# Optimization experiments

Measured on AMD Instinct MI355X. Metric: run time of the kernel, lower is better.

## Reference

```python
import jax, jax.numpy as jnp
import numpy as np

N, NF, INF, NHID = 8192, 128, 128, 16


def _gcn(x, adj, dis, W, b):
    # GraphConvolution: support = x @ W; aggregate with distance-weighted adjacency
    support = x @ W  # [N, out]
    return (adj * dis) @ support + b


def setup_inputs() -> dict:
    key = jax.random.key(0)
    ks = jax.random.split(key, 26)

    def lin(k, i, o):
        kw, kb = jax.random.split(k)
        W = jax.random.uniform(kw, (i, o), jnp.float32, -1.0, 1.0) / np.sqrt(i).astype(np.float32)
        b = jax.random.uniform(kb, (o,), jnp.float32, -1.0, 1.0) / np.sqrt(i).astype(np.float32)
        return W, b

    x = jax.random.normal(ks[0], (N, NF), jnp.float32)
    adj = jax.random.uniform(ks[1], (N, N), jnp.float32)
    dis = jax.random.uniform(ks[2], (N, N), jnp.float32)

    W1, b1 = lin(ks[3], NF, NF)        # linear1
    Wg1, bg1 = lin(ks[4], NF, INF)     # gc1
    Wm1, bm1 = lin(ks[5], INF, 64)     # linear_med1
    Wm2, bm2 = lin(ks[6], 64, 128)     # linear_med2
    Wm3, bm3 = lin(ks[7], 128, 64)     # linear_med3
    Wm4, bm4 = lin(ks[8], 64, 64)      # linear_med4
    Wgh, bgh = lin(ks[9], 64, 64)      # gconv_hidden[0]
    W2, b2 = lin(ks[10], 64, 32)       # linear2
    Wg2, bg2 = lin(ks[11], 32, 32)     # gc2
    W3, b3 = lin(ks[12], 32, NHID)     # linear3

    return dict(x=x, adj=adj, dis=dis, W1=W1, b1=b1, Wg1=Wg1, bg1=bg1,
                Wm1=Wm1, bm1=bm1, Wm2=Wm2, bm2=bm2, Wm3=Wm3, bm3=bm3,
                Wm4=Wm4, bm4=bm4, Wgh=Wgh, bgh=bgh, W2=W2, b2=b2,
                Wg2=Wg2, bg2=bg2, W3=W3, b3=b3)


def reference(x, adj, dis, W1, b1, Wg1, bg1, Wm1, bm1, Wm2, bm2, Wm3, bm3,
              Wm4, bm4, Wgh, bgh, W2, b2, Wg2, bg2, W3, b3):
    lrelu = lambda v: jax.nn.leaky_relu(v, 0.2)
    x0 = _gcn(x @ W1 + b1, adj, dis, Wg1, bg1)
    x0 = lrelu(x0 @ Wm1 + bm1)
    x0 = lrelu(x0 @ Wm2 + bm2)
    x0 = lrelu(x0 @ Wm3 + bm3)
    x0 = jax.nn.relu(x0 @ Wm4 + bm4)
    x_res = x0
    x0 = jax.nn.relu(_gcn(x0, adj, dis, Wgh, bgh) + x_res)  # one hidden gconv layer
    x0 = x0 @ W2 + b2
    x0 = _gcn(x0, adj, dis, Wg2, bg2)
    return x0 @ W3 + b3
```

## Files before the change

kernel.cpp:

```cpp
#include <hip/hip_runtime.h>
#include <hip/hip_bf16.h>

#define NROWS 8192
typedef unsigned short u16;
typedef short bf16x8 __attribute__((ext_vector_type(8)));
typedef short bf16x4 __attribute__((ext_vector_type(4)));
typedef float f32x4 __attribute__((ext_vector_type(4)));

__device__ __forceinline__ u16 f2b(float f) {
    unsigned u = __float_as_uint(f);
    unsigned r = (u + 0x7fffu + ((u >> 16) & 1u)) >> 16;
    return (u16)r;
}
__device__ __forceinline__ float b2f(u16 v) {
    return __uint_as_float(((unsigned)v) << 16);
}

template<int MODE> __device__ __forceinline__ float actf(float v) {
    if constexpr (MODE == 1) return fmaxf(v, 0.f);
    else if constexpr (MODE == 2) return v > 0.f ? v : 0.2f * v;
    else return v;
}

__global__ __launch_bounds__(256) void fold1(
    const float* __restrict__ W1, const float* __restrict__ b1,
    const float* __restrict__ Wg1,
    const float* __restrict__ W2, const float* __restrict__ b2,
    const float* __restrict__ Wg2, float* __restrict__ ws) {
    float* T2 = ws + 9376;
    float* v1 = ws + 11424;
    float* v2 = ws + 11552;
    float* T1 = ws + 16384;
    const int tid = threadIdx.x, b = blockIdx.x;
    if (b < 16) {
        int i = b * 8 + (tid >> 5), j4 = (tid & 31) << 2;
        float4 acc = {0, 0, 0, 0};
        for (int k = 0; k < 128; ++k) {
            float a = W1[i * 128 + k];
            float4 g = *(const float4*)&Wg1[k * 128 + j4];
            acc.x += a * g.x; acc.y += a * g.y; acc.z += a * g.z; acc.w += a * g.w;
        }
        *(float4*)&T1[i * 128 + j4] = acc;
    } else if (b == 16) {
        if (tid < 128) {
            float s = 0;
            for (int k = 0; k < 128; ++k) s += b1[k] * Wg1[k * 128 + tid];
            v1[tid] = s;
        } else if (tid < 160) {
            int j = tid - 128;
            float s = 0;
            for (int k = 0; k < 32; ++k) s += b2[k] * Wg2[k * 32 + j];
            v2[j] = s;
        }
    } else {
        for (int o4 = tid; o4 < 64 * 8; o4 += 256) {
            int i = o4 >> 3, j4 = (o4 & 7) << 2;
            float4 acc = {0, 0, 0, 0};
            for (int k = 0; k < 32; ++k) {
                float a = W2[i * 32 + k];
                float4 g = *(const float4*)&Wg2[k * 32 + j4];
                acc.x += a * g.x; acc.y += a * g.y; acc.z += a * g.z; acc.w += a * g.w;
            }
            *(float4*)&T2[i * 32 + j4] = acc;
        }
    }
}

__global__ __launch_bounds__(256) void fold2(
    const float* __restrict__ Wm1, const float* __restrict__ bm1,
    const float* __restrict__ bg1,
    const float* __restrict__ W3, const float* __restrict__ b3,
    const float* __restrict__ bg2, float* __restrict__ ws) {
    float* WA = ws + 0;
    float* bA = ws + 8192;
    float* cA = ws + 8256;
    float* WB = ws + 8320;
    float* bB = ws + 9344;
    float* cB = ws + 9360;
    const float* T2 = ws + 9376;
    const float* v1 = ws + 11424;
    const float* v2 = ws + 11552;
    const float* T1 = ws + 16384;
    const int tid = threadIdx.x, b = blockIdx.x;
    if (b < 8) {
        int i = b * 16 + (tid >> 4), j4 = (tid & 15) << 2;
        float4 acc = {0, 0, 0, 0};
        for (int k = 0; k < 128; ++k) {
            float a = T1[i * 128 + k];
            float4 g = *(const float4*)&Wm1[k * 64 + j4];
            acc.x += a * g.x; acc.y += a * g.y; acc.z += a * g.z; acc.w += a * g.w;
        }
        *(float4*)&WA[i * 64 + j4] = acc;
    } else if (b == 8) {
        if (tid < 64) {
            float s = 0, c = 0;
            for (int k = 0; k < 128; ++k) {
                s += v1[k] * Wm1[k * 64 + tid];
                c += bg1[k] * Wm1[k * 64 + tid];
            }
            bA[tid] = s; cA[tid] = c + bm1[tid];
        } else if (tid < 80) {
            int j = tid - 64;
            float s = 0, c = 0;
            for (int k = 0; k < 32; ++k) {
                s += v2[k] * W3[k * 16 + j];
                c += bg2[k] * W3[k * 16 + j];
            }
            bB[j] = s; cB[j] = c + b3[j];
        }
    } else {
        int i = tid >> 2, j4 = (tid & 3) << 2;
        float4 acc = {0, 0, 0, 0};
        for (int k = 0; k < 32; ++k) {
            float a = T2[i * 32 + k];
            float4 g = *(const float4*)&W3[k * 16 + j4];
            acc.x += a * g.x; acc.y += a * g.y; acc.z += a * g.z; acc.w += a * g.w;
        }
        *(float4*)&WB[i * 16 + j4] = acc;
    }
}

__global__ __launch_bounds__(256) void gemm_sA(
    const float* __restrict__ in, const float* __restrict__ W,
    const float* __restrict__ bias, u16* __restrict__ St) {
    constexpr int K = 128, M = 64, RB = 32;
    __shared__ float in_t[K][RB + 4];
    __shared__ float w_s[K * M];
    __shared__ float bias_s[M];
    const int tid = threadIdx.x;
    const int b0 = blockIdx.x * RB;
    for (int g = tid; g < RB * (K / 4); g += 256) {
        int r = g / (K / 4), c4 = g % (K / 4);
        float4 v = *(const float4*)&in[(size_t)(b0 + r) * K + c4 * 4];
        in_t[c4 * 4 + 0][r] = v.x;
        in_t[c4 * 4 + 1][r] = v.y;
        in_t[c4 * 4 + 2][r] = v.z;
        in_t[c4 * 4 + 3][r] = v.w;
    }
    for (int g = tid; g < K * M / 4; g += 256)
        ((float4*)w_s)[g] = ((const float4*)W)[g];
    if (tid < M) bias_s[tid] = bias[tid];
    __syncthreads();

    const int tx = tid & 15, ty = tid >> 4;
    const int c0 = tx * 4, r0 = ty * 2;
    float acc[2][4] = {};
    for (int k = 0; k < K; ++k) {
        float a0 = in_t[k][r0], a1 = in_t[k][r0 + 1];
        float4 wv = *(const float4*)&w_s[k * M + c0];
        acc[0][0] += a0 * wv.x; acc[0][1] += a0 * wv.y; acc[0][2] += a0 * wv.z; acc[0][3] += a0 * wv.w;
        acc[1][0] += a1 * wv.x; acc[1][1] += a1 * wv.y; acc[1][2] += a1 * wv.z; acc[1][3] += a1 * wv.w;
    }
#pragma unroll
    for (int m = 0; m < 2; ++m)
#pragma unroll
        for (int n = 0; n < 4; ++n)
            St[(size_t)(c0 + n) * NROWS + (b0 + r0 + m)] = f2b(acc[m][n] + bias_s[c0 + n]);
}

template<int K, int M, int AOUT, int OMODE>
__device__ __forceinline__ void layer_step(
    const float (*pin)[17], const float* __restrict__ w,
    const float* __restrict__ bias,
    float (*pout)[17], float* __restrict__ gout, u16* __restrict__ stout,
    int b0, int tid) {
    constexpr int TXs = M / 4;
    constexpr int TYs = 256 / TXs;
    constexpr int TMs = 16 / TYs;
    static_assert(TMs >= 1, "cfg");
    const int tx = tid % TXs, ty = tid / TXs;
    const int c0 = tx * 4, r0 = ty * TMs;
    float acc[TMs][4] = {};
    for (int k = 0; k < K; ++k) {
        float4 wv = *(const float4*)&w[k * M + c0];
#pragma unroll
        for (int m = 0; m < TMs; ++m) {
            float a = pin[k][r0 + m];
            acc[m][0] += a * wv.x; acc[m][1] += a * wv.y;
            acc[m][2] += a * wv.z; acc[m][3] += a * wv.w;
        }
    }
#pragma unroll
    for (int m = 0; m < TMs; ++m) {
        float v[4];
#pragma unroll
        for (int n = 0; n < 4; ++n) {
            float bv = bias ? bias[c0 + n] : 0.f;
            v[n] = actf<AOUT>(acc[m][n] + bv);
        }
        if constexpr (OMODE != 2) {
#pragma unroll
            for (int n = 0; n < 4; ++n) pout[c0 + n][r0 + m] = v[n];
        }
        if constexpr (OMODE == 1) {
            float4 o = {v[0], v[1], v[2], v[3]};
            *(float4*)&gout[(size_t)(b0 + r0 + m) * M + c0] = o;
        }
        if constexpr (OMODE == 2) {
#pragma unroll
            for (int n = 0; n < 4; ++n)
                stout[(size_t)(c0 + n) * NROWS + (b0 + r0 + m)] = f2b(v[n]);
        }
    }
}

template<int KS>
__global__ __launch_bounds__(256) void med_chain(
    const u16* __restrict__ P, const float* __restrict__ cA,
    const float* __restrict__ Wm2, const float* __restrict__ bm2,
    const float* __restrict__ Wm3, const float* __restrict__ bm3,
    const float* __restrict__ Wm4, const float* __restrict__ bm4,
    const float* __restrict__ Wgh,
    float* __restrict__ h4, u16* __restrict__ St) {
    __shared__ __align__(16) float P0[64][17];
    __shared__ __align__(16) float P1[128][17];
    __shared__ __align__(16) float P2[64][17];
    const int tid = threadIdx.x;
    const int b0 = blockIdx.x * 16;
    constexpr size_t STR = (size_t)NROWS * 64;

    {
        int r = tid >> 4, c4 = (tid & 15) * 4;
        float s[4];
        float4 cv = *(const float4*)&cA[c4];
        s[0] = cv.x; s[1] = cv.y; s[2] = cv.z; s[3] = cv.w;
#pragma unroll
        for (int k = 0; k < KS; ++k) {
            bf16x4 v = *(const bf16x4*)(P + (size_t)k * STR + (size_t)(b0 + r) * 64 + c4);
#pragma unroll
            for (int j = 0; j < 4; ++j) s[j] += b2f((u16)v[j]);
        }
#pragma unroll
        for (int j = 0; j < 4; ++j) P0[c4 + j][r] = actf<2>(s[j]);
    }
    __syncthreads();
    layer_step<64, 128, 2, 0>(P0, Wm2, bm2, P1, nullptr, nullptr, b0, tid);
    __syncthreads();
    layer_step<128, 64, 2, 0>(P1, Wm3, bm3, P2, nullptr, nullptr, b0, tid);
    __syncthreads();
    layer_step<64, 64, 1, 1>(P2, Wm4, bm4, P0, h4, nullptr, b0, tid);
    __syncthreads();
    layer_step<64, 64, 0, 2>(P0, Wgh, nullptr, nullptr, nullptr, St, b0, tid);
}

template<int KS>
__global__ __launch_bounds__(256) void gemm_sB(
    const u16* __restrict__ P, const float* __restrict__ bgh,
    const float* __restrict__ h4,
    const float* __restrict__ WB, const float* __restrict__ bB,
    u16* __restrict__ St) {
    constexpr int K = 64, M = 16, RB = 32;
    __shared__ float in_t[K][RB + 4];
    __shared__ float w_s[K * M];
    const int tid = threadIdx.x;
    const int b0 = blockIdx.x * RB;
    constexpr size_t STR = (size_t)NROWS * 64;

    for (int g = tid; g < RB * 16; g += 256) {
        int r = g >> 4, c4 = (g & 15) * 4;
        float s[4];
        float4 bv = *(const float4*)&bgh[c4];
        s[0] = bv.x; s[1] = bv.y; s[2] = bv.z; s[3] = bv.w;
#pragma unroll
        for (int k = 0; k < KS; ++k) {
            bf16x4 v = *(const bf16x4*)(P + (size_t)k * STR + (size_t)(b0 + r) * 64 + c4);
#pragma unroll
            for (int j = 0; j < 4; ++j) s[j] += b2f((u16)v[j]);
        }
        float4 hv = *(const float4*)&h4[(size_t)(b0 + r) * 64 + c4];
        in_t[c4 + 0][r] = fmaxf(s[0] + hv.x, 0.f);
        in_t[c4 + 1][r] = fmaxf(s[1] + hv.y, 0.f);
        in_t[c4 + 2][r] = fmaxf(s[2] + hv.z, 0.f);
        in_t[c4 + 3][r] = fmaxf(s[3] + hv.w, 0.f);
    }
    for (int g = tid; g < K * M / 4; g += 256)
        ((float4*)w_s)[g] = ((const float4*)WB)[g];
    __syncthreads();

    const int tx = tid & 7, ty = tid >> 3;
    const int c0 = tx * 2, r0 = ty;
    float a0 = 0, a1 = 0;
    for (int k = 0; k < K; ++k) {
        float a = in_t[k][r0];
        a0 += a * w_s[k * M + c0];
        a1 += a * w_s[k * M + c0 + 1];
    }
    St[(size_t)(c0 + 0) * NROWS + (b0 + r0)] = f2b(a0 + bB[c0]);
    St[(size_t)(c0 + 1) * NROWS + (b0 + r0)] = f2b(a1 + bB[c0 + 1]);
}

#define LOADA_F(KC) \
    _Pragma("unroll") for (int r = 0; r < AR4; ++r) { \
        int e4 = r * 256 + tid; \
        size_t g = (size_t)(i0 + (e4 >> 5)) * NROWS + (KC) + (e4 & 31) * 4; \
        rAa[r] = __builtin_nontemporal_load((const f32x4*)(adj + g)); \
        rAd[r] = __builtin_nontemporal_load((const f32x4*)(dis + g)); \
    }

#define STOREA_F(KC) \
    _Pragma("unroll") for (int r = 0; r < AR4; ++r) { \
        int e4 = r * 256 + tid; int row = e4 >> 5; int col = (e4 & 31) * 4; \
        bf16x4 v; \
        _Pragma("unroll") for (int j = 0; j < 4; ++j) v[j] = (short)f2b(rAa[r][j] * rAd[r][j]); \
        if constexpr (MODE == 1) \
            *(bf16x4*)(Abf + (size_t)(i0 + row) * NROWS + (KC) + col) = v; \
        int bo = ((row * BK + col) * 2) ^ ((row & 7) << 4); \
        *(bf16x4*)((char*)As + bo) = v; \
    }

#define LOADA_S(S, KC) \
    _Pragma("unroll") for (int r = 0; r < AR8; ++r) { \
        int e8 = r * 256 + tid; \
        rA##S[r] = *(const bf16x8*)(Abf + (size_t)(i0 + (e8 >> 4)) * NROWS + (KC) + (e8 & 15) * 8); \
    }

#define STOREA_S(S) \
    _Pragma("unroll") for (int r = 0; r < AR8; ++r) { \
        int e8 = r * 256 + tid; int row = e8 >> 4; int col = (e8 & 15) * 8; \
        int bo = ((row * BK + col) * 2) ^ ((row & 7) << 4); \
        *(bf16x8*)((char*)As + bo) = rA##S[r]; \
    }

#define LOADB_S(S, KC) \
    _Pragma("unroll") for (int r = 0; r < BR8; ++r) { \
        int e8 = r * 256 + tid; \
        rB##S[r] = *(const bf16x8*)(St + (size_t)(e8 >> 4) * NROWS + (KC) + (e8 & 15) * 8); \
    }

#define STOREB_S(S) \
    _Pragma("unroll") for (int r = 0; r < BR8; ++r) { \
        int e8 = r * 256 + tid; int c = e8 >> 4; int col = (e8 & 15) * 8; \
        int bo = ((c * BK + col) * 2) ^ ((c & 7) << 4); \
        *(bf16x8*)((char*)Bs + bo) = rB##S[r]; \
    }

#define MFMA_PHASE() \
    _Pragma("unroll") \
    for (int ks = 0; ks < BK; ks += 32) { \
        const int arow = wid * 16 + l15; \
        int ao = ((arow * BK + ks + kb) * 2) ^ ((arow & 7) << 4); \
        bf16x8 af = *(const bf16x8*)((const char*)As + ao); \
        _Pragma("unroll") \
        for (int ct = 0; ct < CT; ++ct) { \
            int bcol = ct * 16 + l15; \
            int bo = ((bcol * BK + ks + kb) * 2) ^ ((bcol & 7) << 4); \
            bf16x8 bf = *(const bf16x8*)((const char*)Bs + bo); \
            acc[ct] = __builtin_amdgcn_mfma_f32_16x16x32_bf16(af, bf, acc[ct], 0, 0, 0); \
        } \
    }

template<int F, int MODE, int KS>
__global__ __launch_bounds__(256) void agg_mfma(
    u16* __restrict__ Abf, const float* __restrict__ adj,
    const float* __restrict__ dis, const u16* __restrict__ St,
    u16* __restrict__ Pout) {
    constexpr int CT = F / 16;
    constexpr int BK = 128;
    constexpr int KCH = NROWS / KS;
    constexpr int NCH = KCH / BK;
    static_assert((NCH & 1) == 0, "even NCH");
    constexpr int AR8 = (64 * BK) / (256 * 8);
    constexpr int AR4 = (64 * BK) / (256 * 4);
    constexpr int BR8 = (F * BK) / (256 * 8);
    __shared__ __align__(16) u16 As[64 * BK];
    __shared__ __align__(16) u16 Bs[F * BK];
    const int tid  = threadIdx.x;
    const int lane = tid & 63;
    const int wid  = tid >> 6;
    const int i0   = blockIdx.x * 64;
    const int ky   = blockIdx.y;
    const int l15  = lane & 15;
    const int kb   = (lane >> 4) * 8;
    const int k0   = ky * KCH;
    f32x4 acc[CT] = {};

    if constexpr (MODE == 0) {
        bf16x8 rAX[AR8], rAY[AR8];
        bf16x8 rBX[BR8], rBY[BR8];
        LOADA_S(X, k0) LOADB_S(X, k0)
        LOADA_S(Y, k0 + BK) LOADB_S(Y, k0 + BK)
        for (int ch = 0; ch < NCH; ch += 2) {
            const int kc = k0 + ch * BK;
            __syncthreads();
            STOREA_S(X) STOREB_S(X)
            __syncthreads();
            if (ch + 2 < NCH) { LOADA_S(X, kc + 2 * BK) LOADB_S(X, kc + 2 * BK) }
            MFMA_PHASE()
            __syncthreads();
            STOREA_S(Y) STOREB_S(Y)
            __syncthreads();
            if (ch + 3 < NCH) { LOADA_S(Y, kc + 3 * BK) LOADB_S(Y, kc + 3 * BK) }
            MFMA_PHASE()
        }
    } else {
        f32x4 rAa[AR4], rAd[AR4];
        bf16x8 rBX[BR8];
        LOADA_F(k0)
        LOADB_S(X, k0)
        for (int ch = 0; ch < NCH; ++ch) {
            const int kc = k0 + ch * BK;
            __syncthreads();
            STOREA_F(kc)
            STOREB_S(X)
            __syncthreads();
            if (ch + 1 < NCH) { LOADA_F(kc + BK) LOADB_S(X, kc + BK) }
            MFMA_PHASE()
        }
    }
    u16* P = Pout + (size_t)ky * ((size_t)NROWS * F);
    const int rb = i0 + wid * 16 + (lane >> 4) * 4;
#pragma unroll
    for (int ct = 0; ct < CT; ++ct)
#pragma unroll
        for (int i = 0; i < 4; ++i)
            P[(size_t)(rb + i) * F + ct * 16 + l15] = f2b(acc[ct][i]);
}
#undef LOADA_F
#undef STOREA_F
#undef LOADA_S
#undef STOREA_S
#undef LOADB_S
#undef STOREB_S
#undef MFMA_PHASE

template<int F, int KS>
__global__ __launch_bounds__(256) void reduce_add(
    const u16* __restrict__ P, const float* __restrict__ bias,
    float* __restrict__ out) {
    constexpr int TOT8 = NROWS * F / 8;
    int i8 = blockIdx.x * 256 + threadIdx.x;
    if (i8 >= TOT8) return;
    constexpr size_t STR = (size_t)NROWS * F;
    float s[8] = {};
#pragma unroll
    for (int k = 0; k < KS; ++k) {
        bf16x8 v = *(const bf16x8*)(P + (size_t)k * STR + (size_t)i8 * 8);
#pragma unroll
        for (int j = 0; j < 8; ++j) s[j] += b2f((u16)v[j]);
    }
    const int c0 = (i8 * 8) % F;
#pragma unroll
    for (int j = 0; j < 8; ++j) s[j] += bias[c0 + j];
    float4* o4 = (float4*)(out + (size_t)i8 * 8);
    float4 oa = {s[0], s[1], s[2], s[3]}, ob = {s[4], s[5], s[6], s[7]};
    o4[0] = oa; o4[1] = ob;
}

extern "C" void kernel_launch(void* const* d_in, const int* in_sizes, int n_in,
                              void* d_out, int out_size, void* d_ws, size_t ws_size,
                              hipStream_t stream) {
    const float* x   = (const float*)d_in[0];
    const float* adj = (const float*)d_in[1];
    const float* dis = (const float*)d_in[2];
    const float* W1  = (const float*)d_in[3];
    const float* b1  = (const float*)d_in[4];
    const float* Wg1 = (const float*)d_in[5];
    const float* bg1 = (const float*)d_in[6];
    const float* Wm1 = (const float*)d_in[7];
    const float* bm1 = (const float*)d_in[8];
    const float* Wm2 = (const float*)d_in[9];
    const float* bm2 = (const float*)d_in[10];
    const float* Wm3 = (const float*)d_in[11];
    const float* bm3 = (const float*)d_in[12];
    const float* Wm4 = (const float*)d_in[13];
    const float* bm4 = (const float*)d_in[14];
    const float* Wgh = (const float*)d_in[15];
    const float* bgh = (const float*)d_in[16];
    const float* W2  = (const float*)d_in[17];
    const float* b2  = (const float*)d_in[18];
    const float* Wg2 = (const float*)d_in[19];
    const float* bg2 = (const float*)d_in[20];
    const float* W3  = (const float*)d_in[21];
    const float* b3  = (const float*)d_in[22];
    float* ws  = (float*)d_ws;
    float* out = (float*)d_out;

    constexpr int KS = 8;
    const size_t ABF_FLOATS = (size_t)NROWS * NROWS / 2;
    const size_t P_FLOATS = (size_t)KS * NROWS * 64 / 2;
    const size_t BASE_FLOATS = 40960 + 262144 + P_FLOATS + 524288;
    const size_t NEED_PRE_BYTES = (ABF_FLOATS + BASE_FLOATS) * 4ULL;
    const bool pre = ws_size >= NEED_PRE_BYTES;

    float* base = ws + (pre ? ABF_FLOATS : 0);
    float* wsW  = base;
    float* St_f = wsW + 40960;
    float* P_f  = St_f + 262144;
    float* h4   = P_f + P_FLOATS;

    u16* Abf = (u16*)ws;
    u16* St  = (u16*)St_f;
    u16* P   = (u16*)P_f;
    const float* WA = wsW + 0;
    const float* bA = wsW + 8192;
    const float* cA = wsW + 8256;
    const float* WB = wsW + 8320;
    const float* bB = wsW + 9344;
    const float* cB = wsW + 9360;

    fold1<<<18, 256, 0, stream>>>(W1, b1, Wg1, W2, b2, Wg2, wsW);
    fold2<<<10, 256, 0, stream>>>(Wm1, bm1, bg1, W3, b3, bg2, wsW);

    gemm_sA<<<256, 256, 0, stream>>>(x, WA, bA, St);
    if (pre) agg_mfma<64, 1, KS><<<dim3(128, KS), 256, 0, stream>>>(Abf, adj, dis, St, P);
    else     agg_mfma<64, 2, KS><<<dim3(128, KS), 256, 0, stream>>>(nullptr, adj, dis, St, P);

    med_chain<KS><<<512, 256, 0, stream>>>(P, cA, Wm2, bm2, Wm3, bm3, Wm4, bm4, Wgh, h4, St);

    if (pre) agg_mfma<64, 0, KS><<<dim3(128, KS), 256, 0, stream>>>(Abf, nullptr, nullptr, St, P);
    else     agg_mfma<64, 2, KS><<<dim3(128, KS), 256, 0, stream>>>(nullptr, adj, dis, St, P);

    gemm_sB<KS><<<256, 256, 0, stream>>>(P, bgh, h4, WB, bB, St);

    if (pre) agg_mfma<16, 0, KS><<<dim3(128, KS), 256, 0, stream>>>(Abf, nullptr, nullptr, St, P);
    else     agg_mfma<16, 2, KS><<<dim3(128, KS), 256, 0, stream>>>(nullptr, adj, dis, St, P);
    reduce_add<16, KS><<<64, 256, 0, stream>>>(P, cB, out);
}
```

Measured before the change: 321.1 us.

## Add warm aggregation kernel using direct global-to-LDS loads with smaller K tiles

Splits the aggregation kernel into a cold variant (fp32 adj*dis with bf16 writeback) and a new warm variant for the later passes that reread the cached bf16 product. The warm kernel uses BK=64 with a double-buffered A tile loaded straight into LDS via global_load_lds when available, with an XOR swizzle applied on the global side. This is meant to cut register staging and VGPR pressure and to overlap A loads with MFMA work. It hardcodes KS=8 in the warm kernel, so it depends on the host KS matching that value.

```diff
diff --git a/kernel.cpp b/kernel.cpp
--- a/kernel.cpp
+++ b/kernel.cpp
@@ -6,6 +6,14 @@
 typedef short bf16x8 __attribute__((ext_vector_type(8)));
 typedef short bf16x4 __attribute__((ext_vector_type(4)));
 typedef float f32x4 __attribute__((ext_vector_type(4)));
+
+#if __has_builtin(__builtin_amdgcn_global_load_lds)
+#define HAS_GLL 1
+typedef __attribute__((address_space(3))) void lds_void;
+typedef __attribute__((address_space(1))) const void glb_cvoid;
+#else
+#define HAS_GLL 0
+#endif
 
 __device__ __forceinline__ u16 f2b(float f) {
     unsigned u = __float_as_uint(f);
@@ -308,36 +316,22 @@
         *(bf16x4*)((char*)As + bo) = v; \
     }
 
-#define LOADA_S(S, KC) \
-    _Pragma("unroll") for (int r = 0; r < AR8; ++r) { \
-        int e8 = r * 256 + tid; \
-        rA##S[r] = *(const bf16x8*)(Abf + (size_t)(i0 + (e8 >> 4)) * NROWS + (KC) + (e8 & 15) * 8); \
-    }
-
-#define STOREA_S(S) \
-    _Pragma("unroll") for (int r = 0; r < AR8; ++r) { \
-        int e8 = r * 256 + tid; int row = e8 >> 4; int col = (e8 & 15) * 8; \
-        int bo = ((row * BK + col) * 2) ^ ((row & 7) << 4); \
-        *(bf16x8*)((char*)As + bo) = rA##S[r]; \
-    }
-
-#define LOADB_S(S, KC) \
+#define LOADB_C(KC) \
     _Pragma("unroll") for (int r = 0; r < BR8; ++r) { \
         int e8 = r * 256 + tid; \
-        rB##S[r] = *(const bf16x8*)(St + (size_t)(e8 >> 4) * NROWS + (KC) + (e8 & 15) * 8); \
-    }
-
-#define STOREB_S(S) \
+        rB[r] = *(const bf16x8*)(St + (size_t)(e8 >> 4) * NROWS + (KC) + (e8 & 15) * 8); \
+    }
+
+#define STOREB_C() \
     _Pragma("unroll") for (int r = 0; r < BR8; ++r) { \
         int e8 = r * 256 + tid; int c = e8 >> 4; int col = (e8 & 15) * 8; \
         int bo = ((c * BK + col) * 2) ^ ((c & 7) << 4); \
-        *(bf16x8*)((char*)Bs + bo) = rB##S[r]; \
-    }
-
-#define MFMA_PHASE() \
+        *(bf16x8*)((char*)Bs + bo) = rB[r]; \
+    }
+
+#define MFMA_C() \
     _Pragma("unroll") \
     for (int ks = 0; ks < BK; ks += 32) { \
-        const int arow = wid * 16 + l15; \
         int ao = ((arow * BK + ks + kb) * 2) ^ ((arow & 7) << 4); \
         bf16x8 af = *(const bf16x8*)((const char*)As + ao); \
         _Pragma("unroll") \
@@ -350,7 +344,7 @@
     }
 
 template<int F, int MODE, int KS>
-__global__ __launch_bounds__(256) void agg_mfma(
+__global__ __launch_bounds__(256) void agg_cold(
     u16* __restrict__ Abf, const float* __restrict__ adj,
     const float* __restrict__ dis, const u16* __restrict__ St,
     u16* __restrict__ Pout) {
@@ -358,8 +352,6 @@
     constexpr int BK = 128;
     constexpr int KCH = NROWS / KS;
     constexpr int NCH = KCH / BK;
-    static_assert((NCH & 1) == 0, "even NCH");
-    constexpr int AR8 = (64 * BK) / (256 * 8);
     constexpr int AR4 = (64 * BK) / (256 * 4);
     constexpr int BR8 = (F * BK) / (256 * 8);
     __shared__ __align__(16) u16 As[64 * BK];
@@ -372,40 +364,21 @@
     const int l15  = lane & 15;
     const int kb   = (lane >> 4) * 8;
     const int k0   = ky * KCH;
+    const int arow = wid * 16 + l15;
     f32x4 acc[CT] = {};
-
-    if constexpr (MODE == 0) {
-        bf16x8 rAX[AR8], rAY[AR8];
-        bf16x8 rBX[BR8], rBY[BR8];
-        LOADA_S(X, k0) LOADB_S(X, k0)
-        LOADA_S(Y, k0 + BK) LOADB_S(Y, k0 + BK)
-        for (int ch = 0; ch < NCH; ch += 2) {
-            const int kc = k0 + ch * BK;
-            __syncthreads();
-            STOREA_S(X) STOREB_S(X)
-            __syncthreads();
-            if (ch + 2 < NCH) { LOADA_S(X, kc + 2 * BK) LOADB_S(X, kc + 2 * BK) }
-            MFMA_PHASE()
-            __syncthreads();
-            STOREA_S(Y) STOREB_S(Y)
-            __syncthreads();
-            if (ch + 3 < NCH) { LOADA_S(Y, kc + 3 * BK) LOADB_S(Y, kc + 3 * BK) }
-            MFMA_PHASE()
-        }
-    } else {
-        f32x4 rAa[AR4], rAd[AR4];
-        bf16x8 rBX[BR8];
-        LOADA_F(k0)
-        LOADB_S(X, k0)
-        for (int ch = 0; ch < NCH; ++ch) {
-            const int kc = k0 + ch * BK;
-            __syncthreads();
-            STOREA_F(kc)
-            STOREB_S(X)
-            __syncthreads();
-            if (ch + 1 < NCH) { LOADA_F(kc + BK) LOADB_S(X, kc + BK) }
-            MFMA_PHASE()
-        }
+    f32x4 rAa[AR4], rAd[AR4];
+    bf16x8 rB[BR8];
+
+    LOADA_F(k0)
+    LOADB_C(k0)
+    for (int ch = 0; ch < NCH; ++ch) {
+        const int kc = k0 + ch * BK;
+        __syncthreads();
+        STOREA_F(kc)
+        STOREB_C()
+        __syncthreads();
+        if (ch + 1 < NCH) { LOADA_F(kc + BK) LOADB_C(kc + BK) }
+        MFMA_C()
     }
     u16* P = Pout + (size_t)ky * ((size_t)NROWS * F);
     const int rb = i0 + wid * 16 + (lane >> 4) * 4;
@@ -417,11 +390,117 @@
 }
 #undef LOADA_F
 #undef STOREA_F
-#undef LOADA_S
-#undef STOREA_S
-#undef LOADB_S
-#undef STOREB_S
-#undef MFMA_PHASE
+
+template<int F>
+__global__ __launch_bounds__(256) void agg_warm(
+    const u16* __restrict__ Abf, const u16* __restrict__ St,
+    u16* __restrict__ Pout) {
+    constexpr int CT = F / 16;
+    constexpr int BK = 64;
+    constexpr int KS = 8;
+    constexpr int KCH = NROWS / KS;
+    constexpr int NCH = KCH / BK;
+    constexpr int BSLOT = F * BK / 8;
+    __shared__ __align__(16) u16 As[2][64 * BK];
+    __shared__ __align__(16) u16 Bs[F * BK];
+    const int tid  = threadIdx.x;
+    const int lane = tid & 63;
+    const int wid  = tid >> 6;
+    const int i0   = blockIdx.x * 64;
+    const int ky   = blockIdx.y;
+    const int l15  = lane & 15;
+    const int kb   = (lane >> 4) * 8;
+    const int k0   = ky * KCH;
+    const int arow = wid * 16 + l15;
+    f32x4 acc[CT] = {};
+
+    const int arl  = lane >> 3;
+    const int agrp = (lane & 7) ^ arl;
+
+#if HAS_GLL
+#define ISSUE_A(BUF, KC) \
+    _Pragma("unroll") for (int i = 0; i < 2; ++i) { \
+        int r0_ = wid * 16 + i * 8; \
+        const u16* gp_ = Abf + (size_t)(i0 + r0_ + arl) * NROWS + (KC) + agrp * 8; \
+        u16* lp_ = &As[BUF][r0_ * BK]; \
+        __builtin_amdgcn_global_load_lds((glb_cvoid*)gp_, (lds_void*)lp_, 16, 0, 0); \
+    }
+#define STOREA_FB(BUF)
+#else
+    bf16x8 rA0, rA1;
+#define ISSUE_A(BUF, KC) { \
+        int e0 = tid, e1 = tid + 256; \
+        rA0 = *(const bf16x8*)(Abf + (size_t)(i0 + (e0 >> 3)) * NROWS + (KC) + (((e0 & 7) ^ ((e0 >> 3) & 7)) * 8)); \
+        rA1 = *(const bf16x8*)(Abf + (size_t)(i0 + (e1 >> 3)) * NROWS + (KC) + (((e1 & 7) ^ ((e1 >> 3) & 7)) * 8)); \
+    }
+#define STOREA_FB(BUF) { \
+        *(bf16x8*)(&As[BUF][(size_t)tid * 8]) = rA0; \
+        *(bf16x8*)(&As[BUF][(size_t)(tid + 256) * 8]) = rA1; \
+    }
+#endif
+
+    bf16x8 rB0, rB1;
+#define LOADB_W(KC) { \
+        if constexpr (F == 64) { \
+            int c0_ = tid >> 3, g0_ = tid & 7; \
+            int c1_ = (tid + 256) >> 3, g1_ = (tid + 256) & 7; \
+            rB0 = *(const bf16x8*)(St + (size_t)c0_ * NROWS + (KC) + ((g0_ ^ (c0_ & 7)) * 8)); \
+            rB1 = *(const bf16x8*)(St + (size_t)c1_ * NROWS + (KC) + ((g1_ ^ (c1_ & 7)) * 8)); \
+        } else { \
+            if (tid < BSLOT) { \
+                int c0_ = tid >> 3, g0_ = tid & 7; \
+                rB0 = *(const bf16x8*)(St + (size_t)c0_ * NROWS + (KC) + ((g0_ ^ (c0_ & 7)) * 8)); \
+            } \
+        } \
+    }
+#define STOREB_W() { \
+        if constexpr (F == 64) { \
+            *(bf16x8*)(&Bs[(size_t)tid * 8]) = rB0; \
+            *(bf16x8*)(&Bs[(size_t)(tid + 256) * 8]) = rB1; \
+        } else { \
+            if (tid < BSLOT) *(bf16x8*)(&Bs[(size_t)tid * 8]) = rB0; \
+        } \
+    }
+
+    ISSUE_A(0, k0)
+    LOADB_W(k0)
+    int cur = 0;
+    for (int ch = 0; ch < NCH; ++ch) {
+        const int kc = k0 + ch * BK;
+        __syncthreads();
+        STOREB_W()
+        STOREA_FB(cur)
+        __syncthreads();
+        if (ch + 1 < NCH) {
+            ISSUE_A(cur ^ 1, kc + BK)
+            LOADB_W(kc + BK)
+        }
+#pragma unroll
+        for (int ks = 0; ks < BK; ks += 32) {
+            int ao = ((arow * BK + ks + kb) * 2) ^ ((arow & 7) << 4);
+            bf16x8 af = *(const bf16x8*)((const char*)As[cur] + ao);
+#pragma unroll
+            for (int ct = 0; ct < CT; ++ct) {
+                int bcol = ct * 16 + l15;
+                int bo = ((bcol * BK + ks + kb) * 2) ^ ((bcol & 7) << 4);
+                bf16x8 bf = *(const bf16x8*)((const char*)Bs + bo);
+                acc[ct] = __builtin_amdgcn_mfma_f32_16x16x32_bf16(af, bf, acc[ct], 0, 0, 0);
+            }
+        }
+        cur ^= 1;
+    }
+#undef ISSUE_A
+#undef STOREA_FB
+#undef LOADB_W
+#undef STOREB_W
+    u16* P = Pout + (size_t)ky * ((size_t)NROWS * F);
+    const int rb = i0 + wid * 16 + (lane >> 4) * 4;
+#pragma unroll
+    for (int ct = 0; ct < CT; ++ct)
+#pragma unroll
+        for (int i = 0; i < 4; ++i)
+            P[(size_t)(rb + i) * F + ct * 16 + l15] = f2b(acc[ct][i]);
+}
 
 template<int F, int KS>
 __global__ __launch_bounds__(256) void reduce_add(
@@ -502,17 +581,17 @@
     fold2<<<10, 256, 0, stream>>>(Wm1, bm1, bg1, W3, b3, bg2, wsW);
 
     gemm_sA<<<256, 256, 0, stream>>>(x, WA, bA, St);
-    if (pre) agg_mfma<64, 1, KS><<<dim3(128, KS), 256, 0, stream>>>(Abf, adj, dis, St, P);
-    else     agg_mfma<64, 2, KS><<<dim3(128, KS), 256, 0, stream>>>(nullptr, adj, dis, St, P);
+    if (pre) agg_cold<64, 1, KS><<<dim3(128, KS), 256, 0, stream>>>(Abf, adj, dis, St, P);
+    else     agg_cold<64, 2, KS><<<dim3(128, KS), 256, 0, stream>>>(nullptr, adj, dis, St, P);
 
     med_chain<KS><<<512, 256, 0, stream>>>(P, cA, Wm2, bm2, Wm3, bm3, Wm4, bm4, Wgh, h4, St);
 
-    if (pre) agg_mfma<64, 0, KS><<<dim3(128, KS), 256, 0, stream>>>(Abf, nullptr, nullptr, St, P);
-    else     agg_mfma<64, 2, KS><<<dim3(128, KS), 256, 0, stream>>>(nullptr, adj, dis, St, P);
+    if (pre) agg_warm<64><<<dim3(128, KS), 256, 0, stream>>>(Abf, St, P);
+    else     agg_cold<64, 2, KS><<<dim3(128, KS), 256, 0, stream>>>(nullptr, adj, dis, St, P);
 
     gemm_sB<KS><<<256, 256, 0, stream>>>(P, bgh, h4, WB, bB, St);
 
-    if (pre) agg_mfma<16, 0, KS><<<dim3(128, KS), 256, 0, stream>>>(Abf, nullptr, nullptr, St, P);
-    else     agg_mfma<16, 2, KS><<<dim3(128, KS), 256, 0, stream>>>(nullptr, adj, dis, St, P);
+    if (pre) agg_warm<16><<<dim3(128, KS), 256, 0, stream>>>(Abf, St, P);
+    else     agg_cold<16, 2, KS><<<dim3(128, KS), 256, 0, stream>>>(nullptr, adj, dis, St, P);
     reduce_add<16, KS><<<64, 256, 0, stream>>>(P, cB, out);
 }
```

Measured after the change: 314.2 us. -2.1%, faster.
